# Performance work log

Measured on AMD Instinct MI355X. Metric: run time of the kernel, lower is better.

## Reference

```python
import jax, jax.numpy as jnp
import numpy as np

NEG_SLOPE = 0.2
EPS = 1e-16  # PyG softmax denominator epsilon


def _gatv2_layer(x, src, dst, n_nodes, W_l, W_r, att, bias):
    """Single-head GATv2Conv (PyG defaults, self loops already in src/dst).
    x: [N, F_in]; src/dst: [E]; W_l/W_r: [F_in, F_out]; att: [F_out]; bias: [F_out].
    """
    x_l = x @ W_l                       # source transform [N, F_out]
    x_r = x @ W_r                       # target transform [N, F_out]
    # per-edge attention logit: a^T LeakyReLU(x_l[j] + x_r[i])
    e = jax.nn.leaky_relu(x_l[src] + x_r[dst], NEG_SLOPE) @ att  # [E]
    # softmax over incoming edges of each destination node
    e_max = jax.ops.segment_max(e, dst, num_segments=n_nodes)    # [N]
    ex = jnp.exp(e - e_max[dst])                                  # [E]
    denom = jax.ops.segment_sum(ex, dst, num_segments=n_nodes)   # [N]
    alpha = ex / (denom[dst] + EPS)                               # [E]
    out = jax.ops.segment_sum(alpha[:, None] * x_l[src], dst, num_segments=n_nodes)
    return out + bias


def setup_inputs() -> dict:
    key = jax.random.key(0)
    N, E = 50000, 800000
    IN, HID, OUT = 128, 64, 64
    ks = jax.random.split(key, 12)
    x = jax.random.normal(ks[0], (N, IN), dtype=jnp.float32)
    edge_index = jax.random.randint(ks[1], (2, E), 0, N, dtype=jnp.int64)
    s1 = float(1.0 / np.sqrt(IN))
    s2 = float(1.0 / np.sqrt(HID))
    return {
        "x": x,
        "edge_index": edge_index,
        "W1_l": jax.random.uniform(ks[2], (IN, HID), jnp.float32, -s1, s1),
        "W1_r": jax.random.uniform(ks[3], (IN, HID), jnp.float32, -s1, s1),
        "att1": jax.random.uniform(ks[4], (HID,), jnp.float32, -s2, s2),
        "b1": jnp.zeros((HID,), jnp.float32),
        "W2_l": jax.random.uniform(ks[5], (HID, OUT), jnp.float32, -s2, s2),
        "W2_r": jax.random.uniform(ks[6], (HID, OUT), jnp.float32, -s2, s2),
        "att2": jax.random.uniform(ks[7], (OUT,), jnp.float32, -s2, s2),
        "b2": jnp.zeros((OUT,), jnp.float32),
    }


def reference(x, edge_index, W1_l, W1_r, att1, b1, W2_l, W2_r, att2, b2):
    n = x.shape[0]
    loop = jnp.arange(n, dtype=edge_index.dtype)
    src = jnp.concatenate([edge_index[0], loop])  # add self loops (PyG default)
    dst = jnp.concatenate([edge_index[1], loop])
    h = _gatv2_layer(x, src, dst, n, W1_l, W1_r, att1, b1)
    h = jax.nn.relu(h)
    out = _gatv2_layer(h, src, dst, n, W2_l, W2_r, att2, b2)
    return out
```

## Files before the change

### kernel.cpp

```cpp
#include <hip/hip_runtime.h>
#include <math.h>

#define NEG_SLOPE 0.2f
#define EPSV 1e-16f
#define NEG_HUGE -1e30f
#define CAP 64
#define GH 512

typedef short short8 __attribute__((ext_vector_type(8)));
typedef float f32x4 __attribute__((ext_vector_type(4)));
typedef unsigned short u16;


__global__ __launch_bounds__(256) void k_wpack(
        const float* __restrict__ W1l, const float* __restrict__ W1r,
        const float* __restrict__ W2l, const float* __restrict__ W2r,
        u16* __restrict__ w1hi, u16* __restrict__ w1lo,
        u16* __restrict__ w2hi, u16* __restrict__ w2lo,
        int* __restrict__ cnt, int CN) {
    const int idx = blockIdx.x * 256 + threadIdx.x;
    const int G = gridDim.x * 256;
    for (int i = idx; i < CN; i += G) cnt[i] = 0;
    const int T1 = 128 * 128, T2 = 64 * 128;
    if (idx >= T1 + T2) return;
    u16 *dhi, *dlo; const float *Wl, *Wr; int li;
    if (idx < T1) { dhi = w1hi; dlo = w1lo; Wl = W1l; Wr = W1r; li = idx; }
    else          { dhi = w2hi; dlo = w2lo; Wl = W2l; Wr = W2r; li = idx - T1; }
    const int j = li & 7, l = (li >> 3) & 63, t = (li >> 9) & 7, c = li >> 12;
    const int k = c * 32 + (l >> 4) * 8 + j;
    const int n = t * 16 + (l & 15);
    const float v = (n < 64) ? Wl[k * 64 + n] : Wr[k * 64 + (n - 64)];
    const unsigned u = __float_as_uint(v);
    dhi[li] = (u16)(u >> 16);
    const float hif = __uint_as_float(u & 0xffff0000u);
    dlo[li] = (u16)(__float_as_uint(v - hif) >> 16);
}

__device__ __forceinline__ void split8(const float* fs, short8& ahi, short8& alo) {
#pragma unroll
    for (int j = 0; j < 8; ++j) {
        const unsigned u = __float_as_uint(fs[j]);
        ahi[j] = (short)(u >> 16);
        const float hif = __uint_as_float(u & 0xffff0000u);
        alo[j] = (short)(__float_as_uint(fs[j] - hif) >> 16);
    }
}

template <int K>
__device__ __forceinline__ void gemm_mfma_tile(const float* __restrict__ X,
                                               const u16* __restrict__ whi,
                                               const u16* __restrict__ wlo,
                                               float* __restrict__ xl,
                                               float* __restrict__ xr,
                                               int N, int tile) {
    const int lane = threadIdx.x & 63;
    const int w = threadIdx.x >> 6;
    const int rowbase = tile * 64 + w * 16;
    const int m = lane & 15, q = lane >> 4;
    int ar = rowbase + m; if (ar > N - 1) ar = N - 1;
    const float* arow = X + (size_t)ar * K + q * 8;
    f32x4 acc[8];
#pragma unroll
    for (int t = 0; t < 8; ++t) acc[t] = (f32x4){0.f, 0.f, 0.f, 0.f};
#pragma unroll
    for (int c = 0; c < K / 32; ++c) {
        const float4 f0 = *(const float4*)(arow + c * 32);
        const float4 f1 = *(const float4*)(arow + c * 32 + 4);
        const float fs[8] = {f0.x, f0.y, f0.z, f0.w, f1.x, f1.y, f1.z, f1.w};
        short8 ahi, alo;
        split8(fs, ahi, alo);
        const u16* bp = whi + ((size_t)(c * 8) * 64 + lane) * 8;
        const u16* bq = wlo + ((size_t)(c * 8) * 64 + lane) * 8;
#pragma unroll
        for (int t = 0; t < 8; ++t) {
            const short8 bhi = *(const short8*)(bp + t * 64 * 8);
            const short8 blo = *(const short8*)(bq + t * 64 * 8);
            acc[t] = __builtin_amdgcn_mfma_f32_16x16x32_bf16(ahi, bhi, acc[t], 0, 0, 0);
            acc[t] = __builtin_amdgcn_mfma_f32_16x16x32_bf16(ahi, blo, acc[t], 0, 0, 0);
            acc[t] = __builtin_amdgcn_mfma_f32_16x16x32_bf16(alo, bhi, acc[t], 0, 0, 0);
        }
    }
#pragma unroll
    for (int t = 0; t < 8; ++t) {
        const int col = t * 16 + m;
        float* dstp = (col < 64) ? (xl + col) : (xr + col - 64);
#pragma unroll
        for (int r = 0; r < 4; ++r) {
            const int row = rowbase + q * 4 + r;
            if (row < N) dstp[(size_t)row * 64] = acc[t][r];
        }
    }
}

template <int K>
__global__ __launch_bounds__(256) void k_hist_gemm(const int* __restrict__ ei, int E,
                                                   int* __restrict__ cnt,
                                                   u16* __restrict__ csrc,
                                                   const float* __restrict__ X,
                                                   const u16* __restrict__ whi,
                                                   const u16* __restrict__ wlo,
                                                   float* __restrict__ xl,
                                                   float* __restrict__ xr,
                                                   int N, int NP) {
    if ((int)blockIdx.x < GH) {
        const int cls = blockIdx.x & 7;
        const int stripe = blockIdx.x >> 3;
        const int NS = GH >> 3;
        const int tid = threadIdx.x;
        const int* srcp = ei;
        const int* dstp = ei + E;
        int* cntc = cnt + cls * NP;
        if ((E & 3) == 0) {
            for (int base = stripe * 1024; base < E; base += NS * 1024) {
                const int e4 = base + tid * 4;
                if (e4 < E) {
                    const int4 d4 = *(const int4*)(dstp + e4);
                    const int4 s4 = *(const int4*)(srcp + e4);
                    if ((d4.x & 7) == cls) {
                        const int slot = atomicAdd(&cntc[d4.x >> 3], 1);
                        csrc[(size_t)d4.x * CAP + slot] = (u16)s4.x;
                    }
                    if ((d4.y & 7) == cls) {
                        const int slot = atomicAdd(&cntc[d4.y >> 3], 1);
                        csrc[(size_t)d4.y * CAP + slot] = (u16)s4.y;
                    }
                    if ((d4.z & 7) == cls) {
                        const int slot = atomicAdd(&cntc[d4.z >> 3], 1);
                        csrc[(size_t)d4.z * CAP + slot] = (u16)s4.z;
                    }
                    if ((d4.w & 7) == cls) {
                        const int slot = atomicAdd(&cntc[d4.w >> 3], 1);
                        csrc[(size_t)d4.w * CAP + slot] = (u16)s4.w;
                    }
                }
            }
        } else {
            for (int base = stripe * 256; base < E; base += NS * 256) {
                const int e = base + tid;
                if (e < E) {
                    const int d = dstp[e];
                    if ((d & 7) == cls) {
                        const int s = srcp[e];
                        const int slot = atomicAdd(&cntc[d >> 3], 1);
                        csrc[(size_t)d * CAP + slot] = (u16)s;
                    }
                }
            }
        }
        for (int k = tid; ((stripe + k * NS) << 3) + cls < N; k += 256) {
            const int d = ((stripe + k * NS) << 3) + cls;
            const int slot = atomicAdd(&cntc[d >> 3], 1);
            csrc[(size_t)d * CAP + slot] = (u16)d;
        }
    } else {
        gemm_mfma_tile<K>(X, whi, wlo, xl, xr, N, blockIdx.x - GH);
    }
}

template <int K>
__global__ __launch_bounds__(256) void k_gemm(const float* __restrict__ X,
                                              const u16* __restrict__ whi,
                                              const u16* __restrict__ wlo,
                                              float* __restrict__ xl,
                                              float* __restrict__ xr, int N) {
    gemm_mfma_tile<K>(X, whi, wlo, xl, xr, N, blockIdx.x);
}

__global__ __launch_bounds__(256) void k_attn(const float* __restrict__ xl,
                                              const float* xr,
                                              const float* __restrict__ att,
                                              const int* __restrict__ cnt,
                                              const u16* __restrict__ csrc,
                                              const float* __restrict__ bias,
                                              float* out, int N, int NP, int relu) {
    const int lane = threadIdx.x & 63;
    const int g = lane >> 4;
    const int i = lane & 15;
    const int dst = blockIdx.x * 4 + (threadIdx.x >> 6);
    if (dst >= N) return;
    const float4 xrv = *(const float4*)(xr + (size_t)dst * 64 + i * 4);
    const float4 aw  = *(const float4*)(att + i * 4);
    const int deg = cnt[(dst & 7) * NP + (dst >> 3)];
    const int sidx = (int)csrc[(size_t)dst * CAP + ((lane < deg) ? lane : 0)];
    float l = 0.0f;
    float4 acc = {0.0f, 0.0f, 0.0f, 0.0f};
    for (int t = 0; t < deg; t += 16) {
        const int s0 = t + g, s1 = t + 4 + g, s2 = t + 8 + g, s3 = t + 12 + g;
        const bool v0 = s0 < deg, v1 = s1 < deg, v2 = s2 < deg, v3 = s3 < deg;
        const int src0 = __shfl(sidx, s0, 64);
        const int src1 = __shfl(sidx, s1, 64);
        const int src2 = __shfl(sidx, s2, 64);
        const int src3 = __shfl(sidx, s3, 64);
        const float4 va = *(const float4*)(xl + (size_t)src0 * 64 + i * 4);
        const float4 vb = *(const float4*)(xl + (size_t)src1 * 64 + i * 4);
        const float4 vc = *(const float4*)(xl + (size_t)src2 * 64 + i * 4);
        const float4 vd = *(const float4*)(xl + (size_t)src3 * 64 + i * 4);
        float t0, p0, p1, p2, p3;
        t0 = va.x + xrv.x; t0 = fmaxf(t0, NEG_SLOPE * t0); p0 = aw.x * t0;
        t0 = va.y + xrv.y; t0 = fmaxf(t0, NEG_SLOPE * t0); p0 = fmaf(aw.y, t0, p0);
        t0 = va.z + xrv.z; t0 = fmaxf(t0, NEG_SLOPE * t0); p0 = fmaf(aw.z, t0, p0);
        t0 = va.w + xrv.w; t0 = fmaxf(t0, NEG_SLOPE * t0); p0 = fmaf(aw.w, t0, p0);
        t0 = vb.x + xrv.x; t0 = fmaxf(t0, NEG_SLOPE * t0); p1 = aw.x * t0;
        t0 = vb.y + xrv.y; t0 = fmaxf(t0, NEG_SLOPE * t0); p1 = fmaf(aw.y, t0, p1);
        t0 = vb.z + xrv.z; t0 = fmaxf(t0, NEG_SLOPE * t0); p1 = fmaf(aw.z, t0, p1);
        t0 = vb.w + xrv.w; t0 = fmaxf(t0, NEG_SLOPE * t0); p1 = fmaf(aw.w, t0, p1);
        t0 = vc.x + xrv.x; t0 = fmaxf(t0, NEG_SLOPE * t0); p2 = aw.x * t0;
        t0 = vc.y + xrv.y; t0 = fmaxf(t0, NEG_SLOPE * t0); p2 = fmaf(aw.y, t0, p2);
        t0 = vc.z + xrv.z; t0 = fmaxf(t0, NEG_SLOPE * t0); p2 = fmaf(aw.z, t0, p2);
        t0 = vc.w + xrv.w; t0 = fmaxf(t0, NEG_SLOPE * t0); p2 = fmaf(aw.w, t0, p2);
        t0 = vd.x + xrv.x; t0 = fmaxf(t0, NEG_SLOPE * t0); p3 = aw.x * t0;
        t0 = vd.y + xrv.y; t0 = fmaxf(t0, NEG_SLOPE * t0); p3 = fmaf(aw.y, t0, p3);
        t0 = vd.z + xrv.z; t0 = fmaxf(t0, NEG_SLOPE * t0); p3 = fmaf(aw.z, t0, p3);
        t0 = vd.w + xrv.w; t0 = fmaxf(t0, NEG_SLOPE * t0); p3 = fmaf(aw.w, t0, p3);
        p0 += __shfl_xor(p0, 1, 64); p1 += __shfl_xor(p1, 1, 64);
        p2 += __shfl_xor(p2, 1, 64); p3 += __shfl_xor(p3, 1, 64);
        p0 += __shfl_xor(p0, 2, 64); p1 += __shfl_xor(p1, 2, 64);
        p2 += __shfl_xor(p2, 2, 64); p3 += __shfl_xor(p3, 2, 64);
        p0 += __shfl_xor(p0, 4, 64); p1 += __shfl_xor(p1, 4, 64);
        p2 += __shfl_xor(p2, 4, 64); p3 += __shfl_xor(p3, 4, 64);
        p0 += __shfl_xor(p0, 8, 64); p1 += __shfl_xor(p1, 8, 64);
        p2 += __shfl_xor(p2, 8, 64); p3 += __shfl_xor(p3, 8, 64);
        const float d0 = __expf(v0 ? p0 : NEG_HUGE);
        const float d1 = __expf(v1 ? p1 : NEG_HUGE);
        const float d2 = __expf(v2 ? p2 : NEG_HUGE);
        const float d3 = __expf(v3 ? p3 : NEG_HUGE);
        l += (d0 + d1) + (d2 + d3);
        acc.x = fmaf(d0, va.x, fmaf(d1, vb.x, fmaf(d2, vc.x, fmaf(d3, vd.x, acc.x))));
        acc.y = fmaf(d0, va.y, fmaf(d1, vb.y, fmaf(d2, vc.y, fmaf(d3, vd.y, acc.y))));
        acc.z = fmaf(d0, va.z, fmaf(d1, vb.z, fmaf(d2, vc.z, fmaf(d3, vd.z, acc.z))));
        acc.w = fmaf(d0, va.w, fmaf(d1, vb.w, fmaf(d2, vc.w, fmaf(d3, vd.w, acc.w))));
    }
#pragma unroll
    for (int o = 16; o <= 32; o <<= 1) {
        l     += __shfl_xor(l, o, 64);
        acc.x += __shfl_xor(acc.x, o, 64);
        acc.y += __shfl_xor(acc.y, o, 64);
        acc.z += __shfl_xor(acc.z, o, 64);
        acc.w += __shfl_xor(acc.w, o, 64);
    }
    if (g == 0) {
        const float4 bv = *(const float4*)(bias + i * 4);
        const float inv = 1.0f / (l + EPSV);
        float4 r;
        r.x = fmaf(acc.x, inv, bv.x);
        r.y = fmaf(acc.y, inv, bv.y);
        r.z = fmaf(acc.z, inv, bv.z);
        r.w = fmaf(acc.w, inv, bv.w);
        if (relu) {
            r.x = fmaxf(r.x, 0.0f); r.y = fmaxf(r.y, 0.0f);
            r.z = fmaxf(r.z, 0.0f); r.w = fmaxf(r.w, 0.0f);
        }
        *(float4*)(out + (size_t)dst * 64 + i * 4) = r;
    }
}


extern "C" void kernel_launch(void* const* d_in, const int* in_sizes, int n_in,
                              void* d_out, int out_size, void* d_ws, size_t ws_size,
                              hipStream_t stream) {
    const float* x    = (const float*)d_in[0];
    const int*   ei   = (const int*)d_in[1];
    const float* W1l  = (const float*)d_in[2];
    const float* W1r  = (const float*)d_in[3];
    const float* att1 = (const float*)d_in[4];
    const float* b1   = (const float*)d_in[5];
    const float* W2l  = (const float*)d_in[6];
    const float* W2r  = (const float*)d_in[7];
    const float* att2 = (const float*)d_in[8];
    const float* b2   = (const float*)d_in[9];

    const int N  = in_sizes[0] / 128;
    const int E  = in_sizes[1] / 2;
    const int NP = (((N + 7) >> 3) + 31) & ~31;

    int* wsi   = (int*)d_ws;
    int* cnt   = wsi;
    u16* csrc  = (u16*)(cnt + 8 * NP);
    u16* w1hi  = csrc + (size_t)N * CAP;
    u16* w1lo  = w1hi + 16384;
    u16* w2hi  = w1lo + 16384;
    u16* w2lo  = w2hi + 8192;
    float* buf1 = (float*)(w2lo + 8192);
    float* buf2 = buf1 + (size_t)N * 64;
    float* fout = (float*)d_out;

    const dim3 b256(256);
    const int gGemm = (N + 63) / 64;
    const int gAttn = (N + 3) / 4;

    k_wpack<<<(128 * 128 + 64 * 128 + 255) / 256, b256, 0, stream>>>(
        W1l, W1r, W2l, W2r, w1hi, w1lo, w2hi, w2lo, cnt, 8 * NP);

    k_hist_gemm<128><<<GH + gGemm, b256, 0, stream>>>(ei, E, cnt, csrc,
                                                      x, w1hi, w1lo, fout, buf1, N, NP);
    k_attn<<<gAttn, b256, 0, stream>>>(fout, buf1, att1, cnt, csrc, b1, buf2, N, NP, 1);

    k_gemm<64><<<gGemm, b256, 0, stream>>>(buf2, w2hi, w2lo, buf1, fout, N);
    k_attn<<<gAttn, b256, 0, stream>>>(buf1, fout, att2, cnt, csrc, b2, fout, N, NP, 0);
}
```

Baseline: 210.9 us.

## Fuse layer-2 projection into layer-1 attention epilogue and vectorize GEMM stores

The second-layer linear transform (x_l and x_r) now runs inside the first attention kernel's epilogue. Each wave stages its 64-wide output row in shared memory and computes both 64-wide projections with FP32 FMAs against a transposed W2 prepared by the pack kernel. This removes the separate layer-2 GEMM launch and the write and read-back of the hidden activations. In exchange, every wave re-reads 32KB of weights from cache and a block barrier is added. The MFMA operands in the layer-1 GEMM are also swapped so each lane holds four contiguous output columns, which turns the strided scalar stores into float4 row stores.

After: 353.5 us. 1.68x slower.

```diff
diff --git a/kernel.cpp b/kernel.cpp
--- a/kernel.cpp
+++ b/kernel.cpp
@@ -16,24 +16,28 @@
         const float* __restrict__ W1l, const float* __restrict__ W1r,
         const float* __restrict__ W2l, const float* __restrict__ W2r,
         u16* __restrict__ w1hi, u16* __restrict__ w1lo,
-        u16* __restrict__ w2hi, u16* __restrict__ w2lo,
+        float* __restrict__ w2t,
         int* __restrict__ cnt, int CN) {
     const int idx = blockIdx.x * 256 + threadIdx.x;
     const int G = gridDim.x * 256;
     for (int i = idx; i < CN; i += G) cnt[i] = 0;
-    const int T1 = 128 * 128, T2 = 64 * 128;
+    const int T1 = 128 * 128, T2 = 128 * 64;
     if (idx >= T1 + T2) return;
-    u16 *dhi, *dlo; const float *Wl, *Wr; int li;
-    if (idx < T1) { dhi = w1hi; dlo = w1lo; Wl = W1l; Wr = W1r; li = idx; }
-    else          { dhi = w2hi; dlo = w2lo; Wl = W2l; Wr = W2r; li = idx - T1; }
-    const int j = li & 7, l = (li >> 3) & 63, t = (li >> 9) & 7, c = li >> 12;
-    const int k = c * 32 + (l >> 4) * 8 + j;
-    const int n = t * 16 + (l & 15);
-    const float v = (n < 64) ? Wl[k * 64 + n] : Wr[k * 64 + (n - 64)];
-    const unsigned u = __float_as_uint(v);
-    dhi[li] = (u16)(u >> 16);
-    const float hif = __uint_as_float(u & 0xffff0000u);
-    dlo[li] = (u16)(__float_as_uint(v - hif) >> 16);
+    if (idx < T1) {
+        const int li = idx;
+        const int j = li & 7, l = (li >> 3) & 63, t = (li >> 9) & 7, c = li >> 12;
+        const int k = c * 32 + (l >> 4) * 8 + j;
+        const int n = t * 16 + (l & 15);
+        const float v = (n < 64) ? W1l[k * 64 + n] : W1r[k * 64 + (n - 64)];
+        const unsigned u = __float_as_uint(v);
+        w1hi[li] = (u16)(u >> 16);
+        const float hif = __uint_as_float(u & 0xffff0000u);
+        w1lo[li] = (u16)(__float_as_uint(v - hif) >> 16);
+    } else {
+        const int li = idx - T1;
+        const int c = li >> 6, k = li & 63;
+        w2t[li] = (c < 64) ? W2l[k * 64 + c] : W2r[k * 64 + (c - 64)];
+    }
 }
 
 __device__ __forceinline__ void split8(const float* fs, short8& ahi, short8& alo) {
@@ -75,19 +79,21 @@
         for (int t = 0; t < 8; ++t) {
             const short8 bhi = *(const short8*)(bp + t * 64 * 8);
             const short8 blo = *(const short8*)(bq + t * 64 * 8);
-            acc[t] = __builtin_amdgcn_mfma_f32_16x16x32_bf16(ahi, bhi, acc[t], 0, 0, 0);
-            acc[t] = __builtin_amdgcn_mfma_f32_16x16x32_bf16(ahi, blo, acc[t], 0, 0, 0);
-            acc[t] = __builtin_amdgcn_mfma_f32_16x16x32_bf16(alo, bhi, acc[t], 0, 0, 0);
-        }
-    }
-#pragma unroll
-    for (int t = 0; t < 8; ++t) {
-        const int col = t * 16 + m;
-        float* dstp = (col < 64) ? (xl + col) : (xr + col - 64);
-#pragma unroll
-        for (int r = 0; r < 4; ++r) {
-            const int row = rowbase + q * 4 + r;
-            if (row < N) dstp[(size_t)row * 64] = acc[t][r];
+            acc[t] = __builtin_amdgcn_mfma_f32_16x16x32_bf16(bhi, ahi, acc[t], 0, 0, 0);
+            acc[t] = __builtin_amdgcn_mfma_f32_16x16x32_bf16(blo, ahi, acc[t], 0, 0, 0);
+            acc[t] = __builtin_amdgcn_mfma_f32_16x16x32_bf16(bhi, alo, acc[t], 0, 0, 0);
+        }
+    }
+    const int row = rowbase + m;
+    if (row < N) {
+#pragma unroll
+        for (int t = 0; t < 8; ++t) {
+            const int colb = t * 16 + q * 4;
+            float4 v;
+            v.x = acc[t][0]; v.y = acc[t][1]; v.z = acc[t][2]; v.w = acc[t][3];
+            float* dstp = (t < 4) ? (xl + (size_t)row * 64 + colb)
+                                  : (xr + (size_t)row * 64 + (colb - 64));
+            *(float4*)dstp = v;
         }
     }
 }
@@ -157,27 +163,24 @@
     }
 }
 
-template <int K>
-__global__ __launch_bounds__(256) void k_gemm(const float* __restrict__ X,
-                                              const u16* __restrict__ whi,
-                                              const u16* __restrict__ wlo,
-                                              float* __restrict__ xl,
-                                              float* __restrict__ xr, int N) {
-    gemm_mfma_tile<K>(X, whi, wlo, xl, xr, N, blockIdx.x);
-}
-
 __global__ __launch_bounds__(256) void k_attn(const float* __restrict__ xl,
                                               const float* xr,
                                               const float* __restrict__ att,
                                               const int* __restrict__ cnt,
                                               const u16* __restrict__ csrc,
                                               const float* __restrict__ bias,
-                                              float* out, int N, int NP, int relu) {
+                                              float* out,
+                                              float* __restrict__ outB,
+                                              const float* __restrict__ w2t,
+                                              int N, int NP, int relu) {
+    __shared__ float hrow[4][64];
     const int lane = threadIdx.x & 63;
+    const int wv = threadIdx.x >> 6;
     const int g = lane >> 4;
     const int i = lane & 15;
-    const int dst = blockIdx.x * 4 + (threadIdx.x >> 6);
-    if (dst >= N) return;
+    const int dst0 = blockIdx.x * 4 + wv;
+    const bool live = dst0 < N;
+    const int dst = live ? dst0 : (N - 1);
     const float4 xrv = *(const float4*)(xr + (size_t)dst * 64 + i * 4);
     const float4 aw  = *(const float4*)(att + i * 4);
     const int deg = cnt[(dst & 7) * NP + (dst >> 3)];
@@ -238,18 +241,39 @@
         acc.z += __shfl_xor(acc.z, o, 64);
         acc.w += __shfl_xor(acc.w, o, 64);
     }
-    if (g == 0) {
-        const float4 bv = *(const float4*)(bias + i * 4);
-        const float inv = 1.0f / (l + EPSV);
-        float4 r;
-        r.x = fmaf(acc.x, inv, bv.x);
-        r.y = fmaf(acc.y, inv, bv.y);
-        r.z = fmaf(acc.z, inv, bv.z);
-        r.w = fmaf(acc.w, inv, bv.w);
-        if (relu) {
-            r.x = fmaxf(r.x, 0.0f); r.y = fmaxf(r.y, 0.0f);
-            r.z = fmaxf(r.z, 0.0f); r.w = fmaxf(r.w, 0.0f);
-        }
+    const float4 bv = *(const float4*)(bias + i * 4);
+    const float inv = 1.0f / (l + EPSV);
+    float4 r;
+    r.x = fmaf(acc.x, inv, bv.x);
+    r.y = fmaf(acc.y, inv, bv.y);
+    r.z = fmaf(acc.z, inv, bv.z);
+    r.w = fmaf(acc.w, inv, bv.w);
+    if (relu) {
+        r.x = fmaxf(r.x, 0.0f); r.y = fmaxf(r.y, 0.0f);
+        r.z = fmaxf(r.z, 0.0f); r.w = fmaxf(r.w, 0.0f);
+    }
+    if (w2t) {
+        if (g == 0) *(float4*)&hrow[wv][i * 4] = r;
+        __syncthreads();
+        const float* hp = hrow[wv];
+        const float* wlp = w2t + (size_t)lane * 64;
+        const float* wrp = w2t + (size_t)(lane + 64) * 64;
+        float sl = 0.0f, sr = 0.0f;
+#pragma unroll
+        for (int k = 0; k < 64; k += 4) {
+            const float4 hv = *(const float4*)(hp + k);
+            const float4 a4 = *(const float4*)(wlp + k);
+            const float4 b4 = *(const float4*)(wrp + k);
+            sl = fmaf(hv.x, a4.x, sl); sl = fmaf(hv.y, a4.y, sl);
+            sl = fmaf(hv.z, a4.z, sl); sl = fmaf(hv.w, a4.w, sl);
+            sr = fmaf(hv.x, b4.x, sr); sr = fmaf(hv.y, b4.y, sr);
+            sr = fmaf(hv.z, b4.z, sr); sr = fmaf(hv.w, b4.w, sr);
+        }
+        if (live) {
+            out[(size_t)dst * 64 + lane]  = sl;
+            outB[(size_t)dst * 64 + lane] = sr;
+        }
+    } else if (g == 0 && live) {
         *(float4*)(out + (size_t)dst * 64 + i * 4) = r;
     }
 }
@@ -278,9 +302,8 @@
     u16* csrc  = (u16*)(cnt + 8 * NP);
     u16* w1hi  = csrc + (size_t)N * CAP;
     u16* w1lo  = w1hi + 16384;
-    u16* w2hi  = w1lo + 16384;
-    u16* w2lo  = w2hi + 8192;
-    float* buf1 = (float*)(w2lo + 8192);
+    float* w2t  = (float*)(w1lo + 16384);
+    float* buf1 = w2t + 8192;
     float* buf2 = buf1 + (size_t)N * 64;
     float* fout = (float*)d_out;
 
@@ -288,13 +311,13 @@
     const int gGemm = (N + 63) / 64;
     const int gAttn = (N + 3) / 4;
 
-    k_wpack<<<(128 * 128 + 64 * 128 + 255) / 256, b256, 0, stream>>>(
-        W1l, W1r, W2l, W2r, w1hi, w1lo, w2hi, w2lo, cnt, 8 * NP);
+    k_wpack<<<(128 * 128 + 128 * 64 + 255) / 256, b256, 0, stream>>>(
+        W1l, W1r, W2l, W2r, w1hi, w1lo, w2t, cnt, 8 * NP);
 
     k_hist_gemm<128><<<GH + gGemm, b256, 0, stream>>>(ei, E, cnt, csrc,
                                                       x, w1hi, w1lo, fout, buf1, N, NP);
-    k_attn<<<gAttn, b256, 0, stream>>>(fout, buf1, att1, cnt, csrc, b1, buf2, N, NP, 1);
-
-    k_gemm<64><<<gGemm, b256, 0, stream>>>(buf2, w2hi, w2lo, buf1, fout, N);
-    k_attn<<<gAttn, b256, 0, stream>>>(buf1, fout, att2, cnt, csrc, b2, fout, N, NP, 0);
-}
+    k_attn<<<gAttn, b256, 0, stream>>>(fout, buf1, att1, cnt, csrc, b1,
+                                       buf1, buf2, w2t, N, NP, 1);
+    k_attn<<<gAttn, b256, 0, stream>>>(buf1, buf2, att2, cnt, csrc, b2,
+                                       fout, nullptr, nullptr, N, NP, 0);
+}
```
